# Kernel optimization log

Measured on AMD Instinct MI355X. Metric: run time of the kernel, lower is better.

## Reference

```python
import jax, jax.numpy as jnp
import numpy as np

A, R = 180, 180  # numAngle, numRho
EPS = 1e-5


def _hough_seg_ids(H, W):
    # Deep Hough Transform binning (Hanqer/deep-hough-transform initTab):
    # irho = int(sqrt(H^2+W^2)+1)/(numRho-1); theta_k = k*pi/numAngle
    irho = int(np.sqrt(H * H + W * W) + 1) / float(R - 1)
    theta = np.arange(A) * (np.pi / A)
    tab_cos = np.cos(theta) / irho  # [A]
    tab_sin = np.sin(theta) / irho
    xs = np.arange(W) - W // 2  # x is width index
    ys = np.arange(H) - H // 2
    r = np.round(tab_cos[:, None, None] * xs[None, None, :]
                 + tab_sin[:, None, None] * ys[None, :, None]).astype(np.int64) + R // 2
    r = np.clip(r, 0, R - 1)
    return jnp.asarray(r.reshape(A, H * W))  # [A, H*W] rho-bin per (angle, pixel)


def _conv_bn_relu(x, w, b, g, beta, m, v, pad):
    y = jax.lax.conv_general_dilated(
        x, w, window_strides=(1, 1), padding=[(pad, pad), (pad, pad)],
        dimension_numbers=('NCHW', 'OIHW', 'NCHW'))
    y = y + b[None, :, None, None]
    scale = g / jnp.sqrt(v + EPS)
    y = (y - m[None, :, None, None]) * scale[None, :, None, None] + beta[None, :, None, None]
    return jax.nn.relu(y)


def _dht(f):
    # f: [N, C, H, W] -> accum [N, C, A, R]
    N, C, H, W = f.shape
    seg = _hough_seg_ids(H, W)  # [A, HW]
    ft = f.reshape(N, C, H * W).transpose(2, 0, 1).reshape(H * W, N * C)  # [HW, N*C]
    acc = jax.vmap(lambda s: jax.ops.segment_sum(ft, s, num_segments=R))(seg)  # [A, R, N*C]
    return acc.reshape(A, R, N, C).transpose(2, 3, 0, 1)  # [N, C, A, R]


def setup_inputs() -> dict:
    key = jax.random.key(0)
    ks = jax.random.split(key, 24)
    N, Ci, dim, H, W = 8, 256, 128, 128, 128
    inp = {
        'x': jax.random.normal(ks[0], (N, Ci, H, W), jnp.float32),
        'w1': jax.random.normal(ks[1], (dim, Ci, 1, 1), jnp.float32) * (1.0 / np.sqrt(Ci)),
        'b1': jax.random.normal(ks[2], (dim,), jnp.float32) * 0.01,
        'g1': jax.random.uniform(ks[3], (dim,), jnp.float32, 0.5, 1.5),
        'be1': jax.random.normal(ks[4], (dim,), jnp.float32) * 0.01,
        'm1': jax.random.normal(ks[5], (dim,), jnp.float32) * 0.1,
        'v1': jax.random.uniform(ks[6], (dim,), jnp.float32, 0.5, 1.5),
        'w2': jax.random.normal(ks[7], (dim, dim, 3, 3), jnp.float32) * (1.0 / np.sqrt(dim * 9)),
        'b2': jax.random.normal(ks[8], (dim,), jnp.float32) * 0.01,
        'g2': jax.random.uniform(ks[9], (dim,), jnp.float32, 0.5, 1.5),
        'be2': jax.random.normal(ks[10], (dim,), jnp.float32) * 0.01,
        'm2': jax.random.normal(ks[11], (dim,), jnp.float32) * 0.1,
        'v2': jax.random.uniform(ks[12], (dim,), jnp.float32, 0.5, 1.5),
        'w3': jax.random.normal(ks[13], (dim, dim, 3, 3), jnp.float32) * (1.0 / np.sqrt(dim * 9)),
        'b3': jax.random.normal(ks[14], (dim,), jnp.float32) * 0.01,
        'g3': jax.random.uniform(ks[15], (dim,), jnp.float32, 0.5, 1.5),
        'be3': jax.random.normal(ks[16], (dim,), jnp.float32) * 0.01,
        'm3': jax.random.normal(ks[17], (dim,), jnp.float32) * 0.1,
        'v3': jax.random.uniform(ks[18], (dim,), jnp.float32, 0.5, 1.5),
    }
    return inp


def reference(x, w1, b1, g1, be1, m1, v1,
              w2, b2, g2, be2, m2, v2,
              w3, b3, g3, be3, m3, v3):
    f = _conv_bn_relu(x, w1, b1, g1, be1, m1, v1, pad=0)   # 1x1 conv + BN + ReLU
    acc = _dht(f)                                           # [N, dim, A, R]
    y = _conv_bn_relu(acc, w2, b2, g2, be2, m2, v2, pad=1)  # 3x3 conv + BN + ReLU
    y = _conv_bn_relu(y, w3, b3, g3, be3, m3, v3, pad=1)
    return y
```

## Files before the change

### kernel.cpp

```cpp
#include <hip/hip_runtime.h>
#include <hip/hip_bf16.h>
#include <math.h>

#define NB 8
#define CI 256
#define CD 128
#define HH 128
#define WW 128
#define HW (HH*WW)
#define AANG 180
#define RRHO 180
#define PADD 182
#define M2 (AANG*RRHO)

typedef __attribute__((ext_vector_type(8))) short short8;
typedef __attribute__((ext_vector_type(8))) _Float16 half8;
typedef __attribute__((ext_vector_type(2))) _Float16 h2;
typedef __attribute__((ext_vector_type(4))) float floatx4;
typedef __attribute__((ext_vector_type(2))) float floatx2;

static __device__ __forceinline__ void async_cp16(const void* g, void* l) {
  __builtin_amdgcn_global_load_lds((const __attribute__((address_space(1))) unsigned int*)g,
                                   (__attribute__((address_space(3))) unsigned int*)l,
                                   16, 0, 0);
}

static __device__ __forceinline__ unsigned short f2bf(float f) {
  unsigned int u = __builtin_bit_cast(unsigned int, f);
  unsigned int r = (u + 0x7fffu + ((u >> 16) & 1u)) >> 16;
  return (unsigned short)r;
}

static __device__ __forceinline__ unsigned short f2h(float f) {
  return __builtin_bit_cast(unsigned short, (_Float16)f);
}

static __device__ __forceinline__ void acc2(float& aL, float& aH, unsigned int u,
                                            h2 eL, h2 eH) {
  h2 hv = __builtin_bit_cast(h2, u);
#if __has_builtin(__builtin_amdgcn_fdot2)
  aL = __builtin_amdgcn_fdot2(hv, eL, aL, false);
  aH = __builtin_amdgcn_fdot2(hv, eH, aH, false);
#else
  aL += (float)hv.x;
  aH += (float)hv.y;
#endif
}

static __device__ __forceinline__ void acc4(float* aL, float* aH, const uint4& v,
                                            h2 eL, h2 eH) {
  acc2(aL[0], aH[0], v.x, eL, eH);
  acc2(aL[1], aH[1], v.y, eL, eH);
  acc2(aL[2], aH[2], v.z, eL, eH);
  acc2(aL[3], aH[3], v.w, eL, eH);
}

__global__ void prep_kernel(const float* __restrict__ w1, const float* __restrict__ w2,
                            const float* __restrict__ w3,
                            const float* b1, const float* g1, const float* be1,
                            const float* m1, const float* v1,
                            const float* b2, const float* g2, const float* be2,
                            const float* m2, const float* v2,
                            const float* b3, const float* g3, const float* be3,
                            const float* m3, const float* v3,
                            unsigned short* __restrict__ wK1, unsigned short* __restrict__ wK2,
                            unsigned short* __restrict__ wK3,
                            float* __restrict__ sc, float* __restrict__ sh) {
  int idx = blockIdx.x * 256 + threadIdx.x;
  if (idx < 32768) {
    wK1[idx] = f2h(w1[idx]);
  } else if (idx < 32768 + 147456) {
    int i = idx - 32768;
    int co = i / 1152, k = i % 1152;
    int dydx = k >> 7, ci = k & 127;
    int dst = (((dydx*2 + (ci >> 6)) * 128 + co) * 64) + (ci & 63);
    wK2[dst] = f2bf(w2[(size_t)(co*128 + ci)*9 + dydx]);
  } else if (idx < 32768 + 2*147456) {
    int i = idx - 32768 - 147456;
    int co = i / 1152, k = i % 1152;
    int dydx = k >> 7, ci = k & 127;
    int dst = (((dydx*2 + (ci >> 6)) * 128 + co) * 64) + (ci & 63);
    wK3[dst] = f2bf(w3[(size_t)(co*128 + ci)*9 + dydx]);
  } else if (idx < 32768 + 2*147456 + 384) {
    int j = idx - 32768 - 2*147456;
    int c = j >> 7, co = j & 127;
    const float* b  = c==0?b1 :(c==1?b2 :b3);
    const float* g  = c==0?g1 :(c==1?g2 :g3);
    const float* be = c==0?be1:(c==1?be2:be3);
    const float* m  = c==0?m1 :(c==1?m2 :m3);
    const float* v  = c==0?v1 :(c==1?v2 :v3);
    float s = g[co] * rsqrtf(v[co] + 1e-5f);
    sc[c*128 + co] = s;
    sh[c*128 + co] = (b[co] - m[co]) * s + be[co];
  }
}

__global__ void histfill_kernel(unsigned int* __restrict__ offs,
                                unsigned short* __restrict__ lst16) {
  int a = blockIdx.x, t = threadIdx.x;
  __shared__ unsigned char segL[HW];
  __shared__ unsigned int h[RRHO];
  __shared__ unsigned int pos[RRHO];
  if (t < RRHO) h[t] = 0;
  __syncthreads();
  double th = (double)a * (M_PI / 180.0);
  double Cc = cos(th) / (182.0 / 179.0);
  double Ss = sin(th) / (182.0 / 179.0);
  for (int p = t; p < HW; p += 256) {
    int x = (p & 127) - 64;
    int y = (p >> 7) - 64;
    int r = (int)rint(Cc * (double)x + Ss * (double)y) + 90;
    r = r < 0 ? 0 : (r > 179 ? 179 : r);
    segL[p] = (unsigned char)r;
    atomicAdd(&h[r], 1u);
  }
  __syncthreads();
  if (t == 0) {
    unsigned int run = 0;
    for (int r = 0; r < RRHO; ++r) {
      pos[r] = run;
      offs[a*192 + r] = run;
      run += h[r];
    }
    offs[a*192 + RRHO] = run;
  }
  __syncthreads();
  int p0 = t * 64;
  for (int i = 0; i < 64; ++i) {
    int p = p0 + i;
    int r = segL[p];
    unsigned int ix = atomicAdd(&pos[r], 1u);
    lst16[(size_t)a*HW + ix] = (unsigned short)p;
  }
}

__global__ void zero_border(uint4* __restrict__ accP, uint4* __restrict__ y2P,
                            unsigned int* __restrict__ qcnt) {
  int idx = blockIdx.x * 256 + threadIdx.x;
  if (idx < 8) qcnt[idx] = 0;
  if (idx >= NB * PADD * PADD) return;
  int rc = idx % (PADD * PADD);
  int row = rc / PADD, col = rc % PADD;
  if (row != 0 && row != PADD-1 && col != 0 && col != PADD-1) return;
  uint4 z = {0u, 0u, 0u, 0u};
  size_t base = (size_t)idx * 16;
  #pragma unroll
  for (int i = 0; i < 16; ++i) { accP[base + i] = z; y2P[base + i] = z; }
}

__global__ __launch_bounds__(256) void conv1_kernel(
    const float* __restrict__ x, const unsigned short* __restrict__ wK,
    const float* __restrict__ sc, const float* __restrict__ sh,
    unsigned short* __restrict__ f) {
  __shared__ short Al[4*128*8];
  __shared__ short Bl[4*128*8];
  int t = threadIdx.x;
  int m0 = blockIdx.x * 128;
  int n = blockIdx.y;
  int lane = t & 63, wv = t >> 6, wm = wv & 1, wn = wv >> 1;
  int mloc = t & 127, octb = t >> 7;
  floatx4 acc[4][4];
  #pragma unroll
  for (int i = 0; i < 4; ++i)
    #pragma unroll
    for (int j = 0; j < 4; ++j) acc[i][j] = (floatx4){0.f, 0.f, 0.f, 0.f};
  const float* xn = x + (size_t)n * CI * HW;
  for (int kc = 0; kc < 8; ++kc) {
    if (kc) __syncthreads();
    #pragma unroll
    for (int j = 0; j < 2; ++j) {
      int oct = octb + 2*j;
      const float* src = xn + (size_t)(kc*32 + oct*8) * HW + m0 + mloc;
      float v[8];
      #pragma unroll
      for (int e = 0; e < 8; ++e) v[e] = src[(size_t)e * HW];
      uint4 pk;
      pk.x = __builtin_bit_cast(unsigned int, __builtin_amdgcn_cvt_pkrtz(v[0], v[1]));
      pk.y = __builtin_bit_cast(unsigned int, __builtin_amdgcn_cvt_pkrtz(v[2], v[3]));
      pk.z = __builtin_bit_cast(unsigned int, __builtin_amdgcn_cvt_pkrtz(v[4], v[5]));
      pk.w = __builtin_bit_cast(unsigned int, __builtin_amdgcn_cvt_pkrtz(v[6], v[7]));
      *reinterpret_cast<uint4*>(&Al[(size_t)(t + 256*j) * 8]) = pk;
    }
    #pragma unroll
    for (int j = 0; j < 2; ++j) {
      int oct = octb + 2*j;
      async_cp16(wK + (size_t)mloc * 256 + kc*32 + oct*8,
                 &Bl[(size_t)((t & 0xFFC0) + 256*j) * 8]);
    }
    __syncthreads();
    int q = lane >> 4, l15 = lane & 15;
    short8 af[4], bfr[4];
    #pragma unroll
    for (int i = 0; i < 4; ++i)
      af[i] = *reinterpret_cast<const short8*>(&Al[((q*128) + wm*64 + i*16 + l15) * 8]);
    #pragma unroll
    for (int j = 0; j < 4; ++j)
      bfr[j] = *reinterpret_cast<const short8*>(&Bl[((q*128) + wn*64 + j*16 + l15) * 8]);
    #pragma unroll
    for (int i = 0; i < 4; ++i)
      #pragma unroll
      for (int j = 0; j < 4; ++j)
        acc[i][j] = __builtin_amdgcn_mfma_f32_16x16x32_f16(
            __builtin_bit_cast(half8, af[i]), __builtin_bit_cast(half8, bfr[j]),
            acc[i][j], 0, 0, 0);
  }
  int q = lane >> 4, l15 = lane & 15;
  #pragma unroll
  for (int j = 0; j < 4; ++j) {
    int co = wn*64 + j*16 + l15;
    float s = sc[co], hb = sh[co];
    #pragma unroll
    for (int i = 0; i < 4; ++i) {
      #pragma unroll
      for (int rg = 0; rg < 4; ++rg) {
        int m = m0 + wm*64 + i*16 + q*4 + rg;
        float v = acc[i][j][rg] * s + hb;
        v = fmaxf(v, 0.f);
        f[((size_t)n * HW + m) * 128 + co] = f2h(v);
      }
    }
  }
}

__global__ __launch_bounds__(512, 8) void dht_kernel(
    const unsigned short* __restrict__ lst16, const unsigned int* __restrict__ offs,
    const unsigned int* __restrict__ f, unsigned int* __restrict__ accP,
    unsigned int* __restrict__ qcnt) {
  __shared__ unsigned short Ls[HW];
  __shared__ unsigned int Os[RRHO + 1];
  __shared__ int sWork;
  int t = threadIdx.x;
  if (t == 0) {
    unsigned int xcd;
    asm volatile("s_getreg_b32 %0, hwreg(HW_REG_XCC_ID, 0, 32)" : "=s"(xcd));
    xcd &= 7u;
    int work = 0;
    for (int k = 0; k < 8; ++k) {
      unsigned int q = (xcd + (unsigned int)k) & 7u;
      unsigned int tk = atomicAdd(&qcnt[q], 1u);
      if (tk < 360u) { work = (int)(q * 360u + tk); break; }
    }
    sWork = work;
  }
  __syncthreads();
  int work = sWork;
  int n = work / 360;
  int rem = work % 360;
  int h = rem / 180;
  int a = rem % 180;
  {
    const uint4* src = (const uint4*)(lst16 + (size_t)a * HW);
    uint4* dst = (uint4*)Ls;
    if (t < RRHO + 1) Os[t] = offs[a*192 + t];
    #pragma unroll
    for (int i = 0; i < 4; ++i) dst[t + 512*i] = src[t + 512*i];
  }
  __syncthreads();
  int w = t >> 6, lane = t & 63;
  int sub = lane >> 3;
  int co  = lane & 7;
  const char* fb = (const char*)(f + (size_t)n * HW * 64);
  unsigned int loff = (unsigned int)(h*32 + co*4) * 4u;
  const h2 eL = {(_Float16)1.0f, (_Float16)0.0f};
  const h2 eH = {(_Float16)0.0f, (_Float16)1.0f};
  for (int r = w; r < RRHO; r += 8) {
    int lo = (int)Os[r];
    int hi = (int)Os[r+1];
    float accL[4], accH[4];
    #pragma unroll
    for (int j = 0; j < 4; ++j) { accL[j] = 0.f; accH[j] = 0.f; }
    while (hi - lo >= 64) {
      unsigned int p0 = Ls[lo + sub];
      unsigned int p1 = Ls[lo + 8 + sub];
      unsigned int p2 = Ls[lo + 16 + sub];
      unsigned int p3 = Ls[lo + 24 + sub];
      unsigned int p4 = Ls[hi - 32 + sub];
      unsigned int p5 = Ls[hi - 24 + sub];
      unsigned int p6 = Ls[hi - 16 + sub];
      unsigned int p7 = Ls[hi - 8 + sub];
      uint4 v0 = *(const uint4*)(fb + ((p0 << 8) + loff));
      uint4 v1 = *(const uint4*)(fb + ((p1 << 8) + loff));
      uint4 v2 = *(const uint4*)(fb + ((p2 << 8) + loff));
      uint4 v3 = *(const uint4*)(fb + ((p3 << 8) + loff));
      uint4 v4 = *(const uint4*)(fb + ((p4 << 8) + loff));
      uint4 v5 = *(const uint4*)(fb + ((p5 << 8) + loff));
      uint4 v6 = *(const uint4*)(fb + ((p6 << 8) + loff));
      uint4 v7 = *(const uint4*)(fb + ((p7 << 8) + loff));
      acc4(accL, accH, v0, eL, eH); acc4(accL, accH, v1, eL, eH);
      acc4(accL, accH, v2, eL, eH); acc4(accL, accH, v3, eL, eH);
      acc4(accL, accH, v4, eL, eH); acc4(accL, accH, v5, eL, eH);
      acc4(accL, accH, v6, eL, eH); acc4(accL, accH, v7, eL, eH);
      lo += 32; hi -= 32;
    }
    for (; lo + 32 <= hi; lo += 32) {
      unsigned int p0 = Ls[lo + sub];
      unsigned int p1 = Ls[lo + 8 + sub];
      unsigned int p2 = Ls[lo + 16 + sub];
      unsigned int p3 = Ls[lo + 24 + sub];
      uint4 v0 = *(const uint4*)(fb + ((p0 << 8) + loff));
      uint4 v1 = *(const uint4*)(fb + ((p1 << 8) + loff));
      uint4 v2 = *(const uint4*)(fb + ((p2 << 8) + loff));
      uint4 v3 = *(const uint4*)(fb + ((p3 << 8) + loff));
      acc4(accL, accH, v0, eL, eH); acc4(accL, accH, v1, eL, eH);
      acc4(accL, accH, v2, eL, eH); acc4(accL, accH, v3, eL, eH);
    }
    for (; lo + 8 <= hi; lo += 8) {
      unsigned int p0 = Ls[lo + sub];
      uint4 v0 = *(const uint4*)(fb + ((p0 << 8) + loff));
      acc4(accL, accH, v0, eL, eH);
    }
    if (lo < hi) {
      int idx = lo + sub;
      int cl = idx < hi ? idx : (hi - 1);
      unsigned int p0 = Ls[cl];
      uint4 v0 = *(const uint4*)(fb + ((p0 << 8) + loff));
      if (idx >= hi) { v0.x = 0; v0.y = 0; v0.z = 0; v0.w = 0; }
      acc4(accL, accH, v0, eL, eH);
    }
    #pragma unroll
    for (int m = 8; m <= 32; m <<= 1) {
      #pragma unroll
      for (int j = 0; j < 4; ++j) {
        accL[j] += __shfl_xor(accL[j], m, 64);
        accH[j] += __shfl_xor(accH[j], m, 64);
      }
    }
    if (sub == 0) {
      uint4 out;
      out.x = (unsigned int)f2bf(accL[0]) | ((unsigned int)f2bf(accH[0]) << 16);
      out.y = (unsigned int)f2bf(accL[1]) | ((unsigned int)f2bf(accH[1]) << 16);
      out.z = (unsigned int)f2bf(accL[2]) | ((unsigned int)f2bf(accH[2]) << 16);
      out.w = (unsigned int)f2bf(accL[3]) | ((unsigned int)f2bf(accH[3]) << 16);
      size_t o = (((size_t)n*PADD + (a+1))*PADD + (r+1))*64 + h*32 + co*4;
      *(uint4*)(accP + o) = out;
    }
  }
}

template<int MODE>
__global__ __launch_bounds__(256, 4) void conv3x3_kernel(
    const unsigned short* __restrict__ inP,
    const unsigned short* __restrict__ wKr,
    const float* __restrict__ sc, const float* __restrict__ sh,
    void* __restrict__ outp) {
  __shared__ short Al[128*64];
  __shared__ short Bl[128*64];
  int t = threadIdx.x;
  int m0 = blockIdx.x * 128;
  int n = blockIdx.y;
  int lane = t & 63, w = t >> 6, wm = w & 1, wn = w >> 1;
  floatx4 acc[4][4];
  #pragma unroll
  for (int i = 0; i < 4; ++i)
    #pragma unroll
    for (int j = 0; j < 4; ++j) acc[i][j] = (floatx4){0.f, 0.f, 0.f, 0.f};

  int srcOct = ((lane & 7) - (lane >> 3)) & 7;
  const unsigned short* rpA[4];
  unsigned int offB[4];
  #pragma unroll
  for (int i = 0; i < 4; ++i) {
    int row = w*32 + i*8 + (lane >> 3);
    int mg = m0 + row; if (mg > M2 - 1) mg = M2 - 1;
    int oa = mg / 180, orr = mg % 180;
    rpA[i] = inP + (((size_t)n*PADD + oa)*PADD + orr)*128 + srcOct*8;
    offB[i] = (unsigned int)(row*64 + srcOct*8);
  }

  for (int step = 0; step < 18; ++step) {
    int dydx = step >> 1, cc2 = step & 1;
    int dy = (dydx * 11) >> 5, dx = dydx - dy*3;
    int doff = (dy*PADD + dx)*128 + cc2*64;
    if (step) __syncthreads();
    #pragma unroll
    for (int i = 0; i < 4; ++i) {
      async_cp16(rpA[i] + doff, &Al[(size_t)((w*4 + i)*64 + lane) * 8]);
      async_cp16(wKr + (size_t)step*8192 + offB[i],
                 &Bl[(size_t)((w*4 + i)*64 + lane) * 8]);
    }
    __syncthreads();
    int q = lane >> 4, l15 = lane & 15;
    #pragma unroll
    for (int kk = 0; kk < 2; ++kk) {
      int o = kk*4 + q;
      int swz = ((o + l15) & 7) * 8;
      short8 rf[4], cf[4];
      #pragma unroll
      for (int i = 0; i < 4; ++i) {
        int addr = (wm*64 + i*16 + l15)*64 + swz;
        rf[i] = *reinterpret_cast<const short8*>(MODE == 1 ? &Al[addr] : &Bl[addr]);
      }
      #pragma unroll
      for (int j = 0; j < 4; ++j) {
        int addr = (wn*64 + j*16 + l15)*64 + swz;
        cf[j] = *reinterpret_cast<const short8*>(MODE == 1 ? &Bl[addr] : &Al[addr]);
      }
      #pragma unroll
      for (int i = 0; i < 4; ++i)
        #pragma unroll
        for (int j = 0; j < 4; ++j)
          acc[i][j] = __builtin_amdgcn_mfma_f32_16x16x32_bf16(rf[i], cf[j], acc[i][j], 0, 0, 0);
    }
  }
  int q = lane >> 4, l15 = lane & 15;
  if (MODE == 1) {
    unsigned short* out = (unsigned short*)outp;
    #pragma unroll
    for (int j = 0; j < 4; ++j) {
      int co = wn*64 + j*16 + l15;
      float s = sc[co], hb = sh[co];
      #pragma unroll
      for (int i = 0; i < 4; ++i) {
        #pragma unroll
        for (int rg = 0; rg < 4; ++rg) {
          int m = m0 + wm*64 + i*16 + q*4 + rg;
          if (m < M2) {
            float v = fmaxf(acc[i][j][rg] * s + hb, 0.f);
            int oa2 = m / 180, or2 = m % 180;
            out[(((size_t)n*PADD + oa2 + 1)*PADD + or2 + 1)*128 + co] = f2bf(v);
          }
        }
      }
    }
  } else {
    float* out = (float*)outp;
    #pragma unroll
    for (int i = 0; i < 4; ++i) {
      #pragma unroll
      for (int rg = 0; rg < 4; ++rg) {
        int co = wm*64 + i*16 + q*4 + rg;
        float s = sc[co], hb = sh[co];
        #pragma unroll
        for (int j = 0; j < 4; ++j) {
          int m = m0 + wn*64 + j*16 + l15;
          if (m < M2) {
            float v = fmaxf(acc[i][j][rg] * s + hb, 0.f);
            out[((size_t)n*128 + co)*M2 + m] = v;
          }
        }
      }
    }
  }
}

extern "C" void kernel_launch(void* const* d_in, const int* in_sizes, int n_in,
                              void* d_out, int out_size, void* d_ws, size_t ws_size,
                              hipStream_t stream) {
  const float* x  = (const float*)d_in[0];
  const float* w1 = (const float*)d_in[1];
  const float* b1 = (const float*)d_in[2];
  const float* g1 = (const float*)d_in[3];
  const float* be1= (const float*)d_in[4];
  const float* m1 = (const float*)d_in[5];
  const float* v1 = (const float*)d_in[6];
  const float* w2 = (const float*)d_in[7];
  const float* b2 = (const float*)d_in[8];
  const float* g2 = (const float*)d_in[9];
  const float* be2= (const float*)d_in[10];
  const float* m2 = (const float*)d_in[11];
  const float* v2 = (const float*)d_in[12];
  const float* w3 = (const float*)d_in[13];
  const float* b3 = (const float*)d_in[14];
  const float* g3 = (const float*)d_in[15];
  const float* be3= (const float*)d_in[16];
  const float* m3 = (const float*)d_in[17];
  const float* v3 = (const float*)d_in[18];

  size_t off = 0;
  char* ws = (char*)d_ws;
  auto alloc = [&](size_t sz) -> void* {
    void* p = ws + off;
    off = (off + sz + 255) & ~(size_t)255;
    return p;
  };
  unsigned short* fbuf = (unsigned short*)alloc((size_t)NB*HW*128*2);
  unsigned short* accP = (unsigned short*)alloc((size_t)NB*PADD*PADD*128*2);
  unsigned short* y2P  = (unsigned short*)alloc((size_t)NB*PADD*PADD*128*2);
  unsigned short* wK1  = (unsigned short*)alloc(32768*2);
  unsigned short* wK2  = (unsigned short*)alloc(147456*2);
  unsigned short* wK3  = (unsigned short*)alloc(147456*2);
  float* sc = (float*)alloc(384*4);
  float* sh = (float*)alloc(384*4);
  unsigned int* offs  = (unsigned int*)alloc((size_t)AANG*192*4);
  unsigned short* lst16 = (unsigned short*)alloc((size_t)AANG*HW*2);
  unsigned int* qcnt  = (unsigned int*)alloc(8*4);

  prep_kernel<<<1282, 256, 0, stream>>>(w1, w2, w3,
      b1, g1, be1, m1, v1, b2, g2, be2, m2, v2, b3, g3, be3, m3, v3,
      wK1, wK2, wK3, sc, sh);
  histfill_kernel<<<AANG, 256, 0, stream>>>(offs, lst16);
  zero_border<<<(NB*PADD*PADD + 255)/256, 256, 0, stream>>>((uint4*)accP, (uint4*)y2P, qcnt);
  conv1_kernel<<<dim3(HW/128, NB), 256, 0, stream>>>(x, wK1, sc, sh, fbuf);
  dht_kernel<<<NB*AANG*2, 512, 0, stream>>>(lst16, offs, (const unsigned int*)fbuf,
                                            (unsigned int*)accP, qcnt);
  conv3x3_kernel<1><<<dim3((M2 + 127)/128, NB), 256, 0, stream>>>(
      accP, wK2, sc + 128, sh + 128, y2P);
  conv3x3_kernel<2><<<dim3((M2 + 127)/128, NB), 256, 0, stream>>>(
      y2P, wK3, sc + 256, sh + 256, d_out);
}
```

Baseline: 727.9 us.

## Merge setup kernels and load conv3x3 weight fragments directly from global

Folds the weight-prep, Hough table build and border-zeroing kernels into one launch to cut launch overhead and serialization. In the 3x3 conv kernels, weight tiles are no longer staged through LDS. Each wave reads its MFMA weight fragments straight from global/L2, which halves LDS use and removes one async copy stream. The trade-off is more scattered global loads per step, and the setup kernel now holds a large shared array in every block, which may lower its occupancy.

```diff
diff --git a/kernel.cpp b/kernel.cpp
--- a/kernel.cpp
+++ b/kernel.cpp
@@ -55,97 +55,98 @@
   acc2(aL[3], aH[3], v.w, eL, eH);
 }
 
-__global__ void prep_kernel(const float* __restrict__ w1, const float* __restrict__ w2,
-                            const float* __restrict__ w3,
-                            const float* b1, const float* g1, const float* be1,
-                            const float* m1, const float* v1,
-                            const float* b2, const float* g2, const float* be2,
-                            const float* m2, const float* v2,
-                            const float* b3, const float* g3, const float* be3,
-                            const float* m3, const float* v3,
-                            unsigned short* __restrict__ wK1, unsigned short* __restrict__ wK2,
-                            unsigned short* __restrict__ wK3,
-                            float* __restrict__ sc, float* __restrict__ sh) {
-  int idx = blockIdx.x * 256 + threadIdx.x;
-  if (idx < 32768) {
-    wK1[idx] = f2h(w1[idx]);
-  } else if (idx < 32768 + 147456) {
-    int i = idx - 32768;
-    int co = i / 1152, k = i % 1152;
-    int dydx = k >> 7, ci = k & 127;
-    int dst = (((dydx*2 + (ci >> 6)) * 128 + co) * 64) + (ci & 63);
-    wK2[dst] = f2bf(w2[(size_t)(co*128 + ci)*9 + dydx]);
-  } else if (idx < 32768 + 2*147456) {
-    int i = idx - 32768 - 147456;
-    int co = i / 1152, k = i % 1152;
-    int dydx = k >> 7, ci = k & 127;
-    int dst = (((dydx*2 + (ci >> 6)) * 128 + co) * 64) + (ci & 63);
-    wK3[dst] = f2bf(w3[(size_t)(co*128 + ci)*9 + dydx]);
-  } else if (idx < 32768 + 2*147456 + 384) {
-    int j = idx - 32768 - 2*147456;
-    int c = j >> 7, co = j & 127;
-    const float* b  = c==0?b1 :(c==1?b2 :b3);
-    const float* g  = c==0?g1 :(c==1?g2 :g3);
-    const float* be = c==0?be1:(c==1?be2:be3);
-    const float* m  = c==0?m1 :(c==1?m2 :m3);
-    const float* v  = c==0?v1 :(c==1?v2 :v3);
-    float s = g[co] * rsqrtf(v[co] + 1e-5f);
-    sc[c*128 + co] = s;
-    sh[c*128 + co] = (b[co] - m[co]) * s + be[co];
-  }
-}
-
-__global__ void histfill_kernel(unsigned int* __restrict__ offs,
-                                unsigned short* __restrict__ lst16) {
-  int a = blockIdx.x, t = threadIdx.x;
-  __shared__ unsigned char segL[HW];
-  __shared__ unsigned int h[RRHO];
-  __shared__ unsigned int pos[RRHO];
-  if (t < RRHO) h[t] = 0;
-  __syncthreads();
-  double th = (double)a * (M_PI / 180.0);
-  double Cc = cos(th) / (182.0 / 179.0);
-  double Ss = sin(th) / (182.0 / 179.0);
-  for (int p = t; p < HW; p += 256) {
-    int x = (p & 127) - 64;
-    int y = (p >> 7) - 64;
-    int r = (int)rint(Cc * (double)x + Ss * (double)y) + 90;
-    r = r < 0 ? 0 : (r > 179 ? 179 : r);
-    segL[p] = (unsigned char)r;
-    atomicAdd(&h[r], 1u);
-  }
-  __syncthreads();
-  if (t == 0) {
-    unsigned int run = 0;
-    for (int r = 0; r < RRHO; ++r) {
-      pos[r] = run;
-      offs[a*192 + r] = run;
-      run += h[r];
-    }
-    offs[a*192 + RRHO] = run;
-  }
-  __syncthreads();
-  int p0 = t * 64;
-  for (int i = 0; i < 64; ++i) {
-    int p = p0 + i;
-    int r = segL[p];
-    unsigned int ix = atomicAdd(&pos[r], 1u);
-    lst16[(size_t)a*HW + ix] = (unsigned short)p;
-  }
-}
-
-__global__ void zero_border(uint4* __restrict__ accP, uint4* __restrict__ y2P,
-                            unsigned int* __restrict__ qcnt) {
-  int idx = blockIdx.x * 256 + threadIdx.x;
-  if (idx < 8) qcnt[idx] = 0;
-  if (idx >= NB * PADD * PADD) return;
-  int rc = idx % (PADD * PADD);
-  int row = rc / PADD, col = rc % PADD;
-  if (row != 0 && row != PADD-1 && col != 0 && col != PADD-1) return;
-  uint4 z = {0u, 0u, 0u, 0u};
-  size_t base = (size_t)idx * 16;
-  #pragma unroll
-  for (int i = 0; i < 16; ++i) { accP[base + i] = z; y2P[base + i] = z; }
+__global__ void setup_kernel(const float* __restrict__ w1, const float* __restrict__ w2,
+                             const float* __restrict__ w3,
+                             const float* b1, const float* g1, const float* be1,
+                             const float* m1, const float* v1,
+                             const float* b2, const float* g2, const float* be2,
+                             const float* m2, const float* v2,
+                             const float* b3, const float* g3, const float* be3,
+                             const float* m3, const float* v3,
+                             unsigned short* __restrict__ wK1, unsigned short* __restrict__ wK2,
+                             unsigned short* __restrict__ wK3,
+                             float* __restrict__ sc, float* __restrict__ sh,
+                             unsigned int* __restrict__ offs,
+                             unsigned short* __restrict__ lst16,
+                             uint4* __restrict__ accP, uint4* __restrict__ y2P,
+                             unsigned int* __restrict__ qcnt) {
+  int b = blockIdx.x, t = threadIdx.x;
+  if (b < 1282) {
+    int idx = b * 256 + t;
+    if (idx < 32768) {
+      wK1[idx] = f2h(w1[idx]);
+    } else if (idx < 32768 + 147456) {
+      int i = idx - 32768;
+      int co = i / 1152, k = i % 1152;
+      int dydx = k >> 7, ci = k & 127;
+      int dst = (((dydx*2 + (ci >> 6)) * 128 + co) * 64) + (ci & 63);
+      wK2[dst] = f2bf(w2[(size_t)(co*128 + ci)*9 + dydx]);
+    } else if (idx < 32768 + 2*147456) {
+      int i = idx - 32768 - 147456;
+      int co = i / 1152, k = i % 1152;
+      int dydx = k >> 7, ci = k & 127;
+      int dst = (((dydx*2 + (ci >> 6)) * 128 + co) * 64) + (ci & 63);
+      wK3[dst] = f2bf(w3[(size_t)(co*128 + ci)*9 + dydx]);
+    } else if (idx < 32768 + 2*147456 + 384) {
+      int j = idx - 32768 - 2*147456;
+      int c = j >> 7, co = j & 127;
+      const float* bb = c==0?b1 :(c==1?b2 :b3);
+      const float* g  = c==0?g1 :(c==1?g2 :g3);
+      const float* be = c==0?be1:(c==1?be2:be3);
+      const float* m  = c==0?m1 :(c==1?m2 :m3);
+      const float* v  = c==0?v1 :(c==1?v2 :v3);
+      float s = g[co] * rsqrtf(v[co] + 1e-5f);
+      sc[c*128 + co] = s;
+      sh[c*128 + co] = (bb[co] - m[co]) * s + be[co];
+    }
+  } else if (b < 1462) {
+    __shared__ unsigned char segL[HW];
+    __shared__ unsigned int h[RRHO];
+    __shared__ unsigned int pos[RRHO];
+    int a = b - 1282;
+    if (t < RRHO) h[t] = 0;
+    __syncthreads();
+    double th = (double)a * (M_PI / 180.0);
+    double Cc = cos(th) / (182.0 / 179.0);
+    double Ss = sin(th) / (182.0 / 179.0);
+    for (int p = t; p < HW; p += 256) {
+      int x = (p & 127) - 64;
+      int y = (p >> 7) - 64;
+      int r = (int)rint(Cc * (double)x + Ss * (double)y) + 90;
+      r = r < 0 ? 0 : (r > 179 ? 179 : r);
+      segL[p] = (unsigned char)r;
+      atomicAdd(&h[r], 1u);
+    }
+    __syncthreads();
+    if (t == 0) {
+      unsigned int run = 0;
+      for (int r = 0; r < RRHO; ++r) {
+        pos[r] = run;
+        offs[a*192 + r] = run;
+        run += h[r];
+      }
+      offs[a*192 + RRHO] = run;
+    }
+    __syncthreads();
+    int p0 = t * 64;
+    for (int i = 0; i < 64; ++i) {
+      int p = p0 + i;
+      int r = segL[p];
+      unsigned int ix = atomicAdd(&pos[r], 1u);
+      lst16[(size_t)a*HW + ix] = (unsigned short)p;
+    }
+  } else {
+    int idx = (b - 1462) * 256 + t;
+    if (idx < 8) qcnt[idx] = 0;
+    if (idx >= NB * PADD * PADD) return;
+    int rc = idx % (PADD * PADD);
+    int row = rc / PADD, col = rc % PADD;
+    if (row != 0 && row != PADD-1 && col != 0 && col != PADD-1) return;
+    uint4 z = {0u, 0u, 0u, 0u};
+    size_t base = (size_t)idx * 16;
+    #pragma unroll
+    for (int i = 0; i < 16; ++i) { accP[base + i] = z; y2P[base + i] = z; }
+  }
 }
 
 __global__ __launch_bounds__(256) void conv1_kernel(
@@ -344,11 +345,11 @@
     const float* __restrict__ sc, const float* __restrict__ sh,
     void* __restrict__ outp) {
   __shared__ short Al[128*64];
-  __shared__ short Bl[128*64];
   int t = threadIdx.x;
   int m0 = blockIdx.x * 128;
   int n = blockIdx.y;
   int lane = t & 63, w = t >> 6, wm = w & 1, wn = w >> 1;
+  int q = lane >> 4, l15 = lane & 15;
   floatx4 acc[4][4];
   #pragma unroll
   for (int i = 0; i < 4; ++i)
@@ -357,15 +358,16 @@
 
   int srcOct = ((lane & 7) - (lane >> 3)) & 7;
   const unsigned short* rpA[4];
-  unsigned int offB[4];
   #pragma unroll
   for (int i = 0; i < 4; ++i) {
     int row = w*32 + i*8 + (lane >> 3);
     int mg = m0 + row; if (mg > M2 - 1) mg = M2 - 1;
     int oa = mg / 180, orr = mg % 180;
     rpA[i] = inP + (((size_t)n*PADD + oa)*PADD + orr)*128 + srcOct*8;
-    offB[i] = (unsigned int)(row*64 + srcOct*8);
-  }
+  }
+  int wside = (MODE == 1) ? wn : wm;
+  int aside = (MODE == 1) ? wm : wn;
+  const unsigned short* wfb = wKr + (size_t)(((wside*64 + l15) * 64) + q*8);
 
   for (int step = 0; step < 18; ++step) {
     int dydx = step >> 1, cc2 = step & 1;
@@ -373,36 +375,31 @@
     int doff = (dy*PADD + dx)*128 + cc2*64;
     if (step) __syncthreads();
     #pragma unroll
-    for (int i = 0; i < 4; ++i) {
+    for (int i = 0; i < 4; ++i)
       async_cp16(rpA[i] + doff, &Al[(size_t)((w*4 + i)*64 + lane) * 8]);
-      async_cp16(wKr + (size_t)step*8192 + offB[i],
-                 &Bl[(size_t)((w*4 + i)*64 + lane) * 8]);
-    }
     __syncthreads();
-    int q = lane >> 4, l15 = lane & 15;
+    const unsigned short* ws = wfb + (size_t)step * 8192;
     #pragma unroll
     for (int kk = 0; kk < 2; ++kk) {
-      int o = kk*4 + q;
-      int swz = ((o + l15) & 7) * 8;
-      short8 rf[4], cf[4];
-      #pragma unroll
-      for (int i = 0; i < 4; ++i) {
-        int addr = (wm*64 + i*16 + l15)*64 + swz;
-        rf[i] = *reinterpret_cast<const short8*>(MODE == 1 ? &Al[addr] : &Bl[addr]);
-      }
-      #pragma unroll
-      for (int j = 0; j < 4; ++j) {
-        int addr = (wn*64 + j*16 + l15)*64 + swz;
-        cf[j] = *reinterpret_cast<const short8*>(MODE == 1 ? &Bl[addr] : &Al[addr]);
+      short8 wf[4], af[4];
+      #pragma unroll
+      for (int x4 = 0; x4 < 4; ++x4)
+        wf[x4] = *reinterpret_cast<const short8*>(ws + x4*1024 + kk*32);
+      int swz = ((kk*4 + q + l15) & 7) * 8;
+      #pragma unroll
+      for (int x4 = 0; x4 < 4; ++x4) {
+        int addr = (aside*64 + x4*16 + l15)*64 + swz;
+        af[x4] = *reinterpret_cast<const short8*>(&Al[addr]);
       }
       #pragma unroll
       for (int i = 0; i < 4; ++i)
         #pragma unroll
         for (int j = 0; j < 4; ++j)
-          acc[i][j] = __builtin_amdgcn_mfma_f32_16x16x32_bf16(rf[i], cf[j], acc[i][j], 0, 0, 0);
-    }
-  }
-  int q = lane >> 4, l15 = lane & 15;
+          acc[i][j] = __builtin_amdgcn_mfma_f32_16x16x32_bf16(
+              MODE == 1 ? af[i] : wf[i], MODE == 1 ? wf[j] : af[j],
+              acc[i][j], 0, 0, 0);
+    }
+  }
   if (MODE == 1) {
     unsigned short* out = (unsigned short*)outp;
     #pragma unroll
@@ -485,11 +482,9 @@
   unsigned short* lst16 = (unsigned short*)alloc((size_t)AANG*HW*2);
   unsigned int* qcnt  = (unsigned int*)alloc(8*4);
 
-  prep_kernel<<<1282, 256, 0, stream>>>(w1, w2, w3,
+  setup_kernel<<<2498, 256, 0, stream>>>(w1, w2, w3,
       b1, g1, be1, m1, v1, b2, g2, be2, m2, v2, b3, g3, be3, m3, v3,
-      wK1, wK2, wK3, sc, sh);
-  histfill_kernel<<<AANG, 256, 0, stream>>>(offs, lst16);
-  zero_border<<<(NB*PADD*PADD + 255)/256, 256, 0, stream>>>((uint4*)accP, (uint4*)y2P, qcnt);
+      wK1, wK2, wK3, sc, sh, offs, lst16, (uint4*)accP, (uint4*)y2P, qcnt);
   conv1_kernel<<<dim3(HW/128, NB), 256, 0, stream>>>(x, wK1, sc, sh, fbuf);
   dht_kernel<<<NB*AANG*2, 512, 0, stream>>>(lst16, offs, (const unsigned int*)fbuf,
                                             (unsigned int*)accP, qcnt);
```

Measured after the change: 890.1 us. 1.22x slower.
